# Performance work log

Measured on AMD Instinct MI355X. Metric: run time of the kernel, lower is better.

## Reference

```python
import jax, jax.numpy as jnp
import numpy as np

N_NODES = 50000
N_EDGES = 800000
IN_DIM = 128
OUT_DIM = 16
N_HEADS = 4
NEG_SLOPE = 0.01  # jax.nn.leaky_relu default, matches original


def setup_inputs() -> dict:
    key = jax.random.key(0)
    k = jax.random.split(key, 8)
    nodes = jax.random.normal(k[0], (N_NODES, IN_DIM), dtype=jnp.float32)
    edges = jax.random.uniform(k[1], (N_NODES, 1), dtype=jnp.float32)  # node-indexed edge attr (edges[senders] in source)
    senders = jax.random.randint(k[2], (N_EDGES,), 0, N_NODES, dtype=jnp.int32)
    receivers = jax.random.randint(k[3], (N_EDGES,), 0, N_NODES, dtype=jnp.int32)
    W = jax.random.normal(k[4], (N_HEADS * OUT_DIM, IN_DIM), dtype=jnp.float32) / np.sqrt(IN_DIM)
    b = jnp.zeros((N_HEADS * OUT_DIM,), dtype=jnp.float32)
    attn_W = jax.random.normal(k[5], (N_HEADS, 2 * OUT_DIM + 1), dtype=jnp.float32) / np.sqrt(2 * OUT_DIM + 1)
    attn_b = jnp.zeros((N_HEADS,), dtype=jnp.float32)
    return dict(nodes=nodes, edges=edges, senders=senders, receivers=receivers,
                W=W, b=b, attn_W=attn_W, attn_b=attn_b)


def _segment_softmax(logits, seg, num_segments):
    # logits: [E, H, 1]; softmax over edges sharing the same receiver
    m = jax.ops.segment_max(logits, seg, num_segments=num_segments)
    e = jnp.exp(logits - m[seg])
    s = jax.ops.segment_sum(e, seg, num_segments=num_segments)
    return e / s[seg]


def reference(nodes, edges, senders, receivers, W, b, attn_W, attn_b):
    n = nodes.shape[0]
    h = (nodes @ W.T + b).reshape(n, N_HEADS, OUT_DIM)       # [N, H, D]
    sent = h[senders]                                        # [E, H, D]
    recv = h[receivers]                                      # [E, H, D]
    sent_e = jnp.tile(edges[senders], (1, N_HEADS))[..., None]  # [E, H, 1]
    feat = jnp.concatenate([sent, recv, sent_e], axis=-1)    # [E, H, 2D+1]
    logits = (jnp.einsum('ehd,hd->eh', feat, attn_W) + attn_b)[..., None]  # [E, H, 1]
    logits = jax.nn.leaky_relu(logits, NEG_SLOPE)
    logits = logits * jnp.sum(sent_e)                        # scalar scaling as in source
    att = _segment_softmax(logits, receivers, n)             # [E, H, 1]
    msg = sent * att                                         # [E, H, D]
    out = jax.ops.segment_sum(msg, receivers, num_segments=n)  # [N, H, D]
    out = jax.nn.leaky_relu(out, NEG_SLOPE)                  # last=False branch
    return out.reshape(n, N_HEADS * OUT_DIM)
```

## Files before the change

### kernel.cpp

```cpp
#include <hip/hip_runtime.h>
#include <math.h>

#define N_NODES 50000
#define N_EDGES 800000
#define IN_DIM 128
#define OUT_DIM 16
#define N_HEADS 4
#define HID 64
#define AW_COLS 33
#define GN 16
#define GEMM_BLK ((N_NODES + GN - 1) / GN)
#define HE 16
#define HBLK ((N_EDGES + 256 * HE - 1) / (256 * HE))
#define MAXDEG 64

__global__ __launch_bounds__(256, 4) void gemm_hist(
    const float* __restrict__ nodes, const float* __restrict__ W,
    const float* __restrict__ b, const float* __restrict__ attn_W,
    const float* __restrict__ attn_b, const float* __restrict__ edges,
    float* __restrict__ h, double* __restrict__ z_src, double* __restrict__ z_dst,
    const int* __restrict__ senders, const int* __restrict__ receivers,
    int* __restrict__ counts, int* __restrict__ srt_padded,
    double* __restrict__ Ssum) {
    __shared__ float sW[HID * IN_DIM];
    __shared__ float sN[GN * IN_DIM];
    int t = threadIdx.x;

    if (blockIdx.x < HBLK) {
        double* red = (double*)sN;
        int base = blockIdx.x * 256 * HE + t;
        double sp = 0.0;
        #pragma unroll
        for (int j = 0; j < HE; ++j) {
            int e = base + j * 256;
            if (e < N_EDGES) {
                int r = receivers[e];
                int rank = atomicAdd(&counts[r], 1);
                if (rank < MAXDEG)
                    srt_padded[r * MAXDEG + rank] = senders[e];
                sp += (double)edges[senders[e]];
            }
        }
        red[t] = sp;
        __syncthreads();
        for (int off = 128; off > 0; off >>= 1) {
            if (t < off) red[t] += red[t + off];
            __syncthreads();
        }
        if (t == 0) atomicAdd(Ssum, red[0]);
    } else {
        for (int i4 = t; i4 < HID * IN_DIM / 4; i4 += 256) {
            int o = i4 >> 5, kq = i4 & 31;
            float4 v = ((const float4*)W)[i4];
            *(float4*)&sW[o * IN_DIM + (((kq + o) & 31) << 2)] = v;
        }
        int node0 = (blockIdx.x - HBLK) * GN;
        for (int i4 = t; i4 < GN * IN_DIM / 4; i4 += 256) {
            int ln = i4 >> 5, kq = i4 & 31;
            float4 v = ((const float4*)nodes)[(long long)(node0 + ln) * (IN_DIM / 4) + kq];
            *(float4*)&sN[ln * IN_DIM + (((kq + ln) & 31) << 2)] = v;
        }
        __syncthreads();

        int w = t >> 6, l = t & 63;
        int og = l & 15;
        int ng = l >> 4;
        int kbase = w * 8;

        double acc[4][4];
        #pragma unroll
        for (int j = 0; j < 4; ++j)
            #pragma unroll
            for (int i = 0; i < 4; ++i) acc[j][i] = 0.0;

        #pragma unroll
        for (int s = 0; s < 8; ++s) {
            int kq = kbase + s;
            float4 wq[4], xq[4];
            #pragma unroll
            for (int j = 0; j < 4; ++j) {
                int o = og + 16 * j;
                wq[j] = *(const float4*)&sW[o * IN_DIM + (((kq + o) & 31) << 2)];
            }
            #pragma unroll
            for (int i = 0; i < 4; ++i) {
                int n = ng + 4 * i;
                xq[i] = *(const float4*)&sN[n * IN_DIM + (((kq + n) & 31) << 2)];
            }
            #pragma unroll
            for (int j = 0; j < 4; ++j) {
                double wx = (double)wq[j].x, wy = (double)wq[j].y;
                double wz = (double)wq[j].z, ww = (double)wq[j].w;
                #pragma unroll
                for (int i = 0; i < 4; ++i) {
                    double nx = (double)xq[i].x, ny = (double)xq[i].y;
                    double nz = (double)xq[i].z, nw = (double)xq[i].w;
                    acc[j][i] += wx * nx; acc[j][i] += wy * ny;
                    acc[j][i] += wz * nz; acc[j][i] += ww * nw;
                }
            }
        }
        __syncthreads();

        double* scr = (double*)sW;
        if (w > 0) {
            double* dst = &scr[((w - 1) * 64 + l) * 17];
            #pragma unroll
            for (int j = 0; j < 4; ++j)
                #pragma unroll
                for (int i = 0; i < 4; ++i) dst[j * 4 + i] = acc[j][i];
        }
        __syncthreads();
        float* h_lds = (float*)sN;
        if (w == 0) {
            #pragma unroll
            for (int j = 0; j < 4; ++j) {
                double bj = (double)b[og + 16 * j];
                #pragma unroll
                for (int i = 0; i < 4; ++i) {
                    double sum = bj + acc[j][i];
                    sum += scr[(0 * 64 + l) * 17 + j * 4 + i];
                    sum += scr[(1 * 64 + l) * 17 + j * 4 + i];
                    sum += scr[(2 * 64 + l) * 17 + j * 4 + i];
                    h_lds[(ng + 4 * i) * HID + og + 16 * j] = (float)sum;
                }
            }
        }
        __syncthreads();

        int half = l >> 5;
        int o2 = l & 31;
        int nwbase = w * 4 + half * 2;
        int hd0 = o2 >> 4, d = o2 & 15;
        int hd1 = hd0 + 2;
        double aw00 = (double)attn_W[hd0 * AW_COLS + d];
        double aw01 = (double)attn_W[hd0 * AW_COLS + OUT_DIM + d];
        double aw10 = (double)attn_W[hd1 * AW_COLS + d];
        double aw11 = (double)attn_W[hd1 * AW_COLS + OUT_DIM + d];
        double wE0 = (double)attn_W[hd0 * AW_COLS + 2 * OUT_DIM];
        double wE1 = (double)attn_W[hd1 * AW_COLS + 2 * OUT_DIM];
        double bb0 = (double)attn_b[hd0], bb1 = (double)attn_b[hd1];
        #pragma unroll
        for (int j = 0; j < 2; ++j) {
            int nl = nwbase + j;
            int n = node0 + nl;
            float hf0 = h_lds[nl * HID + o2];
            float hf1 = h_lds[nl * HID + o2 + 32];
            double c00 = (double)hf0 * aw00;
            double c01 = (double)hf0 * aw01;
            double c10 = (double)hf1 * aw10;
            double c11 = (double)hf1 * aw11;
            #pragma unroll
            for (int k = 1; k <= 8; k <<= 1) {
                c00 += __shfl_xor(c00, k, 64);
                c01 += __shfl_xor(c01, k, 64);
                c10 += __shfl_xor(c10, k, 64);
                c11 += __shfl_xor(c11, k, 64);
            }
            if (d == 0) {
                double se = (double)edges[n];
                z_src[n * N_HEADS + hd0] = c00 + se * wE0;
                z_dst[n * N_HEADS + hd0] = c01 + bb0;
                z_src[n * N_HEADS + hd1] = c10 + se * wE1;
                z_dst[n * N_HEADS + hd1] = c11 + bb1;
            }
        }
        ((float4*)h)[(long long)node0 * (HID / 4) + t] = ((const float4*)h_lds)[t];
    }
}

__global__ __launch_bounds__(256, 8) void node_fused(
    const float* __restrict__ h, const double* __restrict__ z_src,
    const double* __restrict__ z_dst,
    const int* __restrict__ srt_padded, const int* __restrict__ counts,
    const double* __restrict__ Ssum, float* __restrict__ out) {
    int w = threadIdx.x >> 6;
    int lane = threadIdx.x & 63;
    int nA = blockIdx.x * 8 + w * 2;
    int nB = nA + 1;
    int hd = lane >> 4, q = lane & 15;

    int degA = counts[nA]; if (degA > MAXDEG) degA = MAXDEG;
    int degB = counts[nB]; if (degB > MAXDEG) degB = MAXDEG;
    double S = 4.0 * Ssum[0];
    double zdA = z_dst[nA * N_HEADS + hd];
    double zdB = z_dst[nB * N_HEADS + hd];

    int sA[4], sB[4];
    #pragma unroll
    for (int j = 0; j < 4; ++j) {
        int ei = q + 16 * j;
        sA[j] = (ei < degA) ? srt_padded[nA * MAXDEG + ei] : 0;
        sB[j] = (ei < degB) ? srt_padded[nB * MAXDEG + ei] : 0;
    }
    float yA[4], yB[4];
    #pragma unroll
    for (int j = 0; j < 4; ++j) {
        int ei = q + 16 * j;
        yA[j] = -INFINITY;
        yB[j] = -INFINITY;
        if (ei < degA) {
            double yy = z_src[sA[j] * N_HEADS + hd] + zdA;
            yy = yy > 0.0 ? yy : 0.01 * yy;
            yA[j] = (float)yy;
        }
        if (ei < degB) {
            double yy = z_src[sB[j] * N_HEADS + hd] + zdB;
            yy = yy > 0.0 ? yy : 0.01 * yy;
            yB[j] = (float)yy;
        }
    }
    float mA = fmaxf(fmaxf(yA[0], yA[1]), fmaxf(yA[2], yA[3]));
    float mB = fmaxf(fmaxf(yB[0], yB[1]), fmaxf(yB[2], yB[3]));
    #pragma unroll
    for (int k = 1; k <= 8; k <<= 1) {
        mA = fmaxf(mA, __shfl_xor(mA, k, 64));
        mB = fmaxf(mB, __shfl_xor(mB, k, 64));
    }
    float evA[4], evB[4];
    float dA = 0.f, dB = 0.f;
    #pragma unroll
    for (int j = 0; j < 4; ++j) {
        evA[j] = (yA[j] == -INFINITY) ? 0.f
               : __expf((float)(S * ((double)yA[j] - (double)mA)));
        dA += evA[j];
        evB[j] = (yB[j] == -INFINITY) ? 0.f
               : __expf((float)(S * ((double)yB[j] - (double)mB)));
        dB += evB[j];
    }
    #pragma unroll
    for (int k = 1; k <= 8; k <<= 1) {
        dA += __shfl_xor(dA, k, 64);
        dB += __shfl_xor(dB, k, 64);
    }
    float accA = 0.f;
    #pragma unroll
    for (int j = 0; j < 4; ++j) {
        unsigned long long mk = __ballot(evA[j] != 0.f);
        unsigned um = (unsigned)((mk | (mk >> 16) | (mk >> 32) | (mk >> 48)) & 0xFFFFull);
        while (um) {
            int qq = __builtin_ctz(um);
            um &= um - 1;
            int src = (lane & 48) | qq;
            float evv = __shfl(evA[j], src, 64);
            int sj = __shfl(sA[j], src, 64);
            if (evv != 0.f)
                accA = fmaf(evv, h[sj * HID + lane], accA);
        }
    }
    float accB = 0.f;
    #pragma unroll
    for (int j = 0; j < 4; ++j) {
        unsigned long long mk = __ballot(evB[j] != 0.f);
        unsigned um = (unsigned)((mk | (mk >> 16) | (mk >> 32) | (mk >> 48)) & 0xFFFFull);
        while (um) {
            int qq = __builtin_ctz(um);
            um &= um - 1;
            int src = (lane & 48) | qq;
            float evv = __shfl(evB[j], src, 64);
            int sj = __shfl(sB[j], src, 64);
            if (evv != 0.f)
                accB = fmaf(evv, h[sj * HID + lane], accB);
        }
    }
    float rA = (dA > 0.f) ? accA / dA : 0.f;
    float rB = (dB > 0.f) ? accB / dB : 0.f;
    out[nA * HID + lane] = rA > 0.f ? rA : 0.01f * rA;
    out[nB * HID + lane] = rB > 0.f ? rB : 0.01f * rB;
}

static inline char* ws_take(char*& p, size_t bytes) {
    char* cur = p;
    p += (bytes + 255) & ~(size_t)255;
    return cur;
}

extern "C" void kernel_launch(void* const* d_in, const int* in_sizes, int n_in,
                              void* d_out, int out_size, void* d_ws, size_t ws_size,
                              hipStream_t stream) {
    const float* nodes     = (const float*)d_in[0];
    const float* edges     = (const float*)d_in[1];
    const int*   senders   = (const int*)d_in[2];
    const int*   receivers = (const int*)d_in[3];
    const float* W         = (const float*)d_in[4];
    const float* b         = (const float*)d_in[5];
    const float* attn_W    = (const float*)d_in[6];
    const float* attn_b    = (const float*)d_in[7];
    float* out = (float*)d_out;

    char* p = (char*)d_ws;
    float*  h          = (float*)ws_take(p, sizeof(float) * N_NODES * HID);
    double* z_src      = (double*)ws_take(p, sizeof(double) * N_NODES * N_HEADS);
    double* z_dst      = (double*)ws_take(p, sizeof(double) * N_NODES * N_HEADS);
    int*    counts     = (int*)ws_take(p, sizeof(int) * N_NODES);
    char*   zpad       = ws_take(p, 256);
    double* Ssum       = (double*)zpad;
    int*    srt_padded = (int*)ws_take(p, sizeof(int) * (size_t)N_NODES * MAXDEG);

    hipMemsetAsync(counts, 0, ((sizeof(int) * N_NODES + 255) & ~(size_t)255) + 256, stream);

    gemm_hist<<<HBLK + GEMM_BLK, 256, 0, stream>>>(
        nodes, W, b, attn_W, attn_b, edges, h, z_src, z_dst,
        senders, receivers, counts, srt_padded, Ssum);
    node_fused<<<(N_NODES + 7) / 8, 256, 0, stream>>>(
        h, z_src, z_dst, srt_padded, counts, Ssum, out);
}
```

Measured before the change: 155.1 us.

## Read W from global, double node tile, split K across two waves

```diff
diff --git a/kernel.cpp b/kernel.cpp
--- a/kernel.cpp
+++ b/kernel.cpp
@@ -8,13 +8,16 @@
 #define N_HEADS 4
 #define HID 64
 #define AW_COLS 33
-#define GN 16
+#define GN 32
 #define GEMM_BLK ((N_NODES + GN - 1) / GN)
 #define HE 16
 #define HBLK ((N_EDGES + 256 * HE - 1) / (256 * HE))
 #define MAXDEG 64
 
-__global__ __launch_bounds__(256, 4) void gemm_hist(
+#define SCR_DOUBLES (2 * 64 * 17)
+#define SMEM_DOUBLES 3200
+
+__global__ __launch_bounds__(256, 6) void gemm_hist(
     const float* __restrict__ nodes, const float* __restrict__ W,
     const float* __restrict__ b, const float* __restrict__ attn_W,
     const float* __restrict__ attn_b, const float* __restrict__ edges,
@@ -22,12 +25,12 @@
     const int* __restrict__ senders, const int* __restrict__ receivers,
     int* __restrict__ counts, int* __restrict__ srt_padded,
     double* __restrict__ Ssum) {
-    __shared__ float sW[HID * IN_DIM];
-    __shared__ float sN[GN * IN_DIM];
+    __shared__ double smem_d[SMEM_DOUBLES];
+    float* sN = (float*)smem_d;
     int t = threadIdx.x;
 
     if (blockIdx.x < HBLK) {
-        double* red = (double*)sN;
+        double* red = smem_d;
         int base = blockIdx.x * 256 * HE + t;
         double sp = 0.0;
         #pragma unroll
@@ -49,23 +52,21 @@
         }
         if (t == 0) atomicAdd(Ssum, red[0]);
     } else {
-        for (int i4 = t; i4 < HID * IN_DIM / 4; i4 += 256) {
-            int o = i4 >> 5, kq = i4 & 31;
-            float4 v = ((const float4*)W)[i4];
-            *(float4*)&sW[o * IN_DIM + (((kq + o) & 31) << 2)] = v;
-        }
         int node0 = (blockIdx.x - HBLK) * GN;
         for (int i4 = t; i4 < GN * IN_DIM / 4; i4 += 256) {
             int ln = i4 >> 5, kq = i4 & 31;
-            float4 v = ((const float4*)nodes)[(long long)(node0 + ln) * (IN_DIM / 4) + kq];
+            int n = node0 + ln;
+            float4 v = (n < N_NODES) ? ((const float4*)nodes)[(long long)n * (IN_DIM / 4) + kq]
+                                     : make_float4(0.f, 0.f, 0.f, 0.f);
             *(float4*)&sN[ln * IN_DIM + (((kq + ln) & 31) << 2)] = v;
         }
         __syncthreads();
 
         int w = t >> 6, l = t & 63;
+        int g = w >> 1, kw = w & 1;
         int og = l & 15;
         int ng = l >> 4;
-        int kbase = w * 8;
+        int kbase = kw * 16;
 
         double acc[4][4];
         #pragma unroll
@@ -73,19 +74,18 @@
             #pragma unroll
             for (int i = 0; i < 4; ++i) acc[j][i] = 0.0;
 
+        const float4* Wq = (const float4*)W;
         #pragma unroll
-        for (int s = 0; s < 8; ++s) {
+        for (int s = 0; s < 16; ++s) {
             int kq = kbase + s;
             float4 wq[4], xq[4];
             #pragma unroll
-            for (int j = 0; j < 4; ++j) {
-                int o = og + 16 * j;
-                wq[j] = *(const float4*)&sW[o * IN_DIM + (((kq + o) & 31) << 2)];
-            }
+            for (int j = 0; j < 4; ++j)
+                wq[j] = Wq[(og + 16 * j) * (IN_DIM / 4) + kq];
             #pragma unroll
             for (int i = 0; i < 4; ++i) {
-                int n = ng + 4 * i;
-                xq[i] = *(const float4*)&sN[n * IN_DIM + (((kq + n) & 31) << 2)];
+                int ln = g * 16 + ng + 4 * i;
+                xq[i] = *(const float4*)&sN[ln * IN_DIM + (((kq + ln) & 31) << 2)];
             }
             #pragma unroll
             for (int j = 0; j < 4; ++j) {
@@ -102,27 +102,25 @@
         }
         __syncthreads();
 
-        double* scr = (double*)sW;
-        if (w > 0) {
-            double* dst = &scr[((w - 1) * 64 + l) * 17];
+        double* scr = smem_d;
+        float* h_lds = (float*)(smem_d + SCR_DOUBLES);
+        if (kw == 1) {
+            double* dst = &scr[(g * 64 + l) * 17];
             #pragma unroll
             for (int j = 0; j < 4; ++j)
                 #pragma unroll
                 for (int i = 0; i < 4; ++i) dst[j * 4 + i] = acc[j][i];
         }
         __syncthreads();
-        float* h_lds = (float*)sN;
-        if (w == 0) {
+        if (kw == 0) {
+            const double* src = &scr[(g * 64 + l) * 17];
             #pragma unroll
             for (int j = 0; j < 4; ++j) {
                 double bj = (double)b[og + 16 * j];
                 #pragma unroll
                 for (int i = 0; i < 4; ++i) {
-                    double sum = bj + acc[j][i];
-                    sum += scr[(0 * 64 + l) * 17 + j * 4 + i];
-                    sum += scr[(1 * 64 + l) * 17 + j * 4 + i];
-                    sum += scr[(2 * 64 + l) * 17 + j * 4 + i];
-                    h_lds[(ng + 4 * i) * HID + og + 16 * j] = (float)sum;
+                    double sum = bj + acc[j][i] + src[j * 4 + i];
+                    h_lds[(g * 16 + ng + 4 * i) * HID + og + 16 * j] = (float)sum;
                 }
             }
         }
@@ -130,7 +128,7 @@
 
         int half = l >> 5;
         int o2 = l & 31;
-        int nwbase = w * 4 + half * 2;
+        int nwbase = w * 8 + half * 4;
         int hd0 = o2 >> 4, d = o2 & 15;
         int hd1 = hd0 + 2;
         double aw00 = (double)attn_W[hd0 * AW_COLS + d];
@@ -141,7 +139,7 @@
         double wE1 = (double)attn_W[hd1 * AW_COLS + 2 * OUT_DIM];
         double bb0 = (double)attn_b[hd0], bb1 = (double)attn_b[hd1];
         #pragma unroll
-        for (int j = 0; j < 2; ++j) {
+        for (int j = 0; j < 4; ++j) {
             int nl = nwbase + j;
             int n = node0 + nl;
             float hf0 = h_lds[nl * HID + o2];
@@ -157,7 +155,7 @@
                 c10 += __shfl_xor(c10, k, 64);
                 c11 += __shfl_xor(c11, k, 64);
             }
-            if (d == 0) {
+            if (n < N_NODES && d == 0) {
                 double se = (double)edges[n];
                 z_src[n * N_HEADS + hd0] = c00 + se * wE0;
                 z_dst[n * N_HEADS + hd0] = c01 + bb0;
@@ -165,7 +163,14 @@
                 z_dst[n * N_HEADS + hd1] = c11 + bb1;
             }
         }
-        ((float4*)h)[(long long)node0 * (HID / 4) + t] = ((const float4*)h_lds)[t];
+        {
+            const float4* hq = (const float4*)h_lds;
+            int i0 = t, i1 = t + 256;
+            if (node0 + (i0 >> 4) < N_NODES)
+                ((float4*)h)[(long long)node0 * (HID / 4) + i0] = hq[i0];
+            if (node0 + (i1 >> 4) < N_NODES)
+                ((float4*)h)[(long long)node0 * (HID / 4) + i1] = hq[i1];
+        }
     }
 }
 
```

Result: slower. 259.3 us (+67.2%).
